# Performance work log

Measured on AMD Instinct MI355X. Metric: run time of the kernel, lower is better.

## Reference

```python
import jax, jax.numpy as jnp
import numpy as np

PAST = 15        # sum(num_classes[:-1])
NC = 20          # sum(num_classes)
ALPHA = 0.99
IGNORE = 255


def setup_inputs() -> dict:
    key = jax.random.key(0)
    k1, k2, k3, k4, k5, k6 = jax.random.split(key, 6)
    B, C, H, W = 8, NC, 512, 512
    logit = jax.random.normal(k1, (B, C, H, W), dtype=jnp.float32)
    # ema_prob is used as probabilities (gathered & compared to thresholds)
    ema_prob = jax.nn.softmax(jax.random.normal(k2, (B, C, H, W), dtype=jnp.float32), axis=1)
    ema_thresh = jax.random.uniform(k3, (NC,), dtype=jnp.float32, minval=0.2, maxval=0.8)
    real_labels = jax.random.randint(k4, (B, H, W), 0, NC, dtype=jnp.int64)
    # sprinkle ignore pixels (255) like real segmentation masks
    real_labels = jnp.where(jax.random.uniform(k5, (B, H, W)) < 0.1, IGNORE, real_labels)
    moving_prob_avg = jax.random.uniform(k6, (NC,), dtype=jnp.float32)
    return {"logit": logit, "ema_prob": ema_prob, "ema_thresh": ema_thresh,
            "real_labels": real_labels, "moving_prob_avg": moving_prob_avg}


def reference(logit, ema_prob, ema_thresh, real_labels, moving_prob_avg):
    # --- pseudo-labels from current model (detached softmax) ---
    logit_prob = jax.nn.softmax(jax.lax.stop_gradient(logit), axis=1)  # [B,C,H,W]
    labels = jnp.argmax(logit_prob[:, :PAST], axis=1)                   # [B,H,W]
    labels = jnp.where(real_labels >= PAST, real_labels, labels)
    idx = jnp.where(real_labels == IGNORE, 0, labels)
    scores = jnp.take_along_axis(logit_prob, idx[:, None], axis=1)[:, 0]  # [B,H,W]

    # --- per-class mean of scores + EMA update of moving_prob_avg ---
    flat_lab = labels.reshape(-1)
    flat_sc = scores.reshape(-1)
    seg = jnp.where(flat_lab == IGNORE, NC, flat_lab)  # route ignored to extra bucket
    sums = jax.ops.segment_sum(flat_sc, seg, num_segments=NC + 1)[:NC]
    counts = jax.ops.segment_sum(jnp.ones_like(flat_sc), seg, num_segments=NC + 1)[:NC]
    means = sums / jnp.maximum(counts, 1.0)
    mpa = moving_prob_avg  # numpy buffer in torch (no grad)
    new_mpa = jnp.where(counts > 0,
                        jnp.where(mpa == -1.0, means, (1.0 - ALPHA) * means + ALPHA * mpa),
                        mpa)

    # --- EMA-teacher pseudo labels + threshold mask ---
    ema_labels = jnp.argmax(ema_prob[:, :PAST], axis=1)
    ema_labels = jnp.where(real_labels >= PAST, real_labels, ema_labels)
    eidx = jnp.where(real_labels == IGNORE, 0, ema_labels)
    ema_scores = jnp.take_along_axis(ema_prob, eidx[:, None], axis=1)[:, 0]
    valid_cls = ema_labels < NC  # 255 never matches any class in the torch loop
    thr = ema_thresh[jnp.clip(ema_labels, 0, NC - 1)]
    ema_mask = valid_cls & (ema_scores >= thr)
    dynamic_labels = jnp.where(ema_mask, ema_labels, IGNORE)  # [B,H,W]

    # --- masked cross-entropy with per-class reweighting ---
    logp = jax.nn.log_softmax(logit, axis=1)
    cidx = jnp.clip(dynamic_labels, 0, NC - 1)
    losses = -jnp.take_along_axis(logp, cidx[:, None], axis=1)[:, 0]
    valid = dynamic_labels != IGNORE
    mult = jnp.where(valid, 1.0 - new_mpa[cidx], 1.0)
    losses = losses * jax.lax.stop_gradient(mult)  # multiplier is a host scalar in torch
    vs = valid.astype(losses.dtype)
    return jnp.sum(losses * vs) / jnp.sum(vs)
```

## Files before the change

### kernel.cpp

```cpp
#include <hip/hip_runtime.h>
#include <math.h>


#define PASTC 15
#define NCC   20
#define IGN   255
#define HW2   262144
#define ALPHAF 0.99f
#define DPF   4

__device__ __forceinline__ void gld_lds16(const float* g, void* l) {
    __builtin_amdgcn_global_load_lds(
        (const __attribute__((address_space(1))) void*)g,
        (__attribute__((address_space(3))) void*)l,
        16, 0, 0);
}

__global__ __launch_bounds__(256) void dl_main(
    const float* __restrict__ logit,
    const float* __restrict__ ema,
    const float* __restrict__ thresh,
    const int*   __restrict__ real,
    float*       __restrict__ ws)
{
    __shared__ float4 s_e[DPF][256];
    __shared__ float4 s_l[DPF][256];
    __shared__ float  s_acc[61];
    __shared__ float  s_thr[NCC];

    const int tid = threadIdx.x;
    if (tid < 61) s_acc[tid] = 0.0f;
    if (tid < NCC) s_thr[tid] = thresh[tid];
    __syncthreads();

    const int t  = blockIdx.x * 256 + tid;
    const int p0 = t << 2;
    const int b  = p0 >> 18;
    const int s  = p0 & (HW2 - 1);
    const size_t base = (((size_t)(b * NCC)) << 18) + (size_t)s;
    const float* eb = ema   + base;
    const float* lb = logit + base;
    const int wbase = tid & ~63;

    const int4 rl4 = *reinterpret_cast<const int4*>(real + p0);
    const int rl[4] = {rl4.x, rl4.y, rl4.z, rl4.w};

    int   cap_ch[4];
    float se[4], x_m15[4], esel[4], xsel[4];
    int   arg15[4], earg[4];
#pragma unroll
    for (int j = 0; j < 4; ++j) {
        cap_ch[j] = (rl[j] == IGN) ? 0 : (rl[j] >= PASTC ? rl[j] : -1);
        se[j] = 0.0f; x_m15[j] = -INFINITY; esel[j] = -INFINITY;
        xsel[j] = 0.0f; arg15[j] = 0; earg[j] = 0;
    }

#pragma unroll
    for (int c = 0; c < DPF; ++c) {
        gld_lds16(eb + ((size_t)c << 18), &s_e[c][wbase]);
        gld_lds16(lb + ((size_t)c << 18), &s_l[c][wbase]);
    }

#pragma unroll
    for (int c = 0; c < NCC; ++c) {
        const int slot = c & (DPF - 1);
        const int vm = (c + DPF < NCC) ? 2 * (DPF - 1) : 2 * (NCC - 1 - c);
        asm volatile("s_waitcnt vmcnt(%0)" :: "n"(vm) : "memory");
        __builtin_amdgcn_sched_barrier(0);

        const float4 ve4 = s_e[slot][tid];
        const float4 vl4 = s_l[slot][tid];
        const float ev[4] = {ve4.x, ve4.y, ve4.z, ve4.w};
        const float xv[4] = {vl4.x, vl4.y, vl4.z, vl4.w};
#pragma unroll
        for (int j = 0; j < 4; ++j) {
            const float x = xv[j];
            se[j] += __expf(x);
            if (c < PASTC) {
                const bool gl = x > x_m15[j];
                x_m15[j] = gl ? x : x_m15[j];
                arg15[j] = gl ? c : arg15[j];
            }
            const bool upd = (cap_ch[j] < 0)
                               ? (c < PASTC && ev[j] > esel[j])
                               : (c == cap_ch[j]);
            esel[j] = upd ? ev[j] : esel[j];
            earg[j] = upd ? c    : earg[j];
            xsel[j] = upd ? x    : xsel[j];
        }

        if (c + DPF < NCC) {
            gld_lds16(eb + ((size_t)(c + DPF) << 18), &s_e[slot][wbase]);
            gld_lds16(lb + ((size_t)(c + DPF) << 18), &s_l[slot][wbase]);
        }
    }

    float vcnt = 0.0f;
#pragma unroll
    for (int j = 0; j < 4; ++j) {
        const float lse = __logf(se[j]);
        if (rl[j] != IGN) {
            const int   lab  = (rl[j] >= PASTC) ? rl[j] : arg15[j];
            const float sval = (rl[j] >= PASTC) ? xsel[j] : x_m15[j];
            const float prob = __expf(sval - lse);
            atomicAdd(&s_acc[lab], prob);
            atomicAdd(&s_acc[20 + lab], 1.0f);
        }
        const int  el    = (rl[j] >= PASTC) ? rl[j] : earg[j];
        const float th   = s_thr[el < NCC ? el : (NCC - 1)];
        const bool valid = (el < NCC) && (esel[j] >= th);
        if (valid) {
            atomicAdd(&s_acc[40 + el], lse - xsel[j]);
        }
        const unsigned long long bm = __ballot(valid);
        if ((tid & 63) == 0) vcnt += (float)__popcll(bm);
    }
    if ((tid & 63) == 0) atomicAdd(&s_acc[60], vcnt);

    __syncthreads();
    if (tid < 61) atomicAdd(&ws[tid], s_acc[tid]);
}

__global__ void dl_final(const float* __restrict__ ws,
                         const float* __restrict__ mpa,
                         float*       __restrict__ out)
{
    if (threadIdx.x == 0 && blockIdx.x == 0) {
        float acc = 0.0f;
        for (int c = 0; c < NCC; ++c) {
            const float ssum = ws[c];
            const float cnt  = ws[20 + c];
            const float lsum = ws[40 + c];
            const float m    = mpa[c];
            const float mean = ssum / fmaxf(cnt, 1.0f);
            const float nm   = (cnt > 0.0f)
                                 ? ((m == -1.0f) ? mean
                                                 : (1.0f - ALPHAF) * mean + ALPHAF * m)
                                 : m;
            acc += lsum * (1.0f - nm);
        }
        out[0] = acc / ws[60];
    }
}

extern "C" void kernel_launch(void* const* d_in, const int* in_sizes, int n_in,
                              void* d_out, int out_size, void* d_ws, size_t ws_size,
                              hipStream_t stream) {
    const float* logit  = (const float*)d_in[0];
    const float* ema    = (const float*)d_in[1];
    const float* thresh = (const float*)d_in[2];
    const int*   real   = (const int*)d_in[3];
    const float* mpa    = (const float*)d_in[4];
    float* out = (float*)d_out;
    float* ws  = (float*)d_ws;

    hipMemsetAsync(ws, 0, 64 * sizeof(float), stream);

    dl_main<<<2048, 256, 0, stream>>>(logit, ema, thresh, real, ws);
    dl_final<<<1, 64, 0, stream>>>(ws, mpa, out);
}
```

Baseline: 364.5 us.

## Split ema and logit passes with direct vector loads, drop LDS prefetch pipeline

Replaces the hand-built global_load_lds ring buffer, which interleaved ema and logit channels, with two sequential passes of plain float4 global loads. The first pass computes the ema argmax and selected value. The second computes the logit sum-exp, argmax and selected logit using the known ema label. Labels and ema scores are parked in LDS to cut register pressure, and launch bounds request 8 blocks per CU. The goal is higher occupancy so the compiler and hardware can hide memory latency with more waves. The cost is losing the explicit prefetch depth.

```diff
diff --git a/kernel.cpp b/kernel.cpp
--- a/kernel.cpp
+++ b/kernel.cpp
@@ -7,26 +7,18 @@
 #define IGN   255
 #define HW2   262144
 #define ALPHAF 0.99f
-#define DPF   4
 
-__device__ __forceinline__ void gld_lds16(const float* g, void* l) {
-    __builtin_amdgcn_global_load_lds(
-        (const __attribute__((address_space(1))) void*)g,
-        (__attribute__((address_space(3))) void*)l,
-        16, 0, 0);
-}
-
-__global__ __launch_bounds__(256) void dl_main(
+__global__ __launch_bounds__(256, 8) void dl_main(
     const float* __restrict__ logit,
     const float* __restrict__ ema,
     const float* __restrict__ thresh,
     const int*   __restrict__ real,
     float*       __restrict__ ws)
 {
-    __shared__ float4 s_e[DPF][256];
-    __shared__ float4 s_l[DPF][256];
     __shared__ float  s_acc[61];
     __shared__ float  s_thr[NCC];
+    __shared__ int4   s_rl[256];
+    __shared__ float4 s_es[256];
 
     const int tid = threadIdx.x;
     if (tid < 61) s_acc[tid] = 0.0f;
@@ -40,75 +32,94 @@
     const size_t base = (((size_t)(b * NCC)) << 18) + (size_t)s;
     const float* eb = ema   + base;
     const float* lb = logit + base;
-    const int wbase = tid & ~63;
 
     const int4 rl4 = *reinterpret_cast<const int4*>(real + p0);
+    s_rl[tid] = rl4;
     const int rl[4] = {rl4.x, rl4.y, rl4.z, rl4.w};
 
-    int   cap_ch[4];
-    float se[4], x_m15[4], esel[4], xsel[4];
-    int   arg15[4], earg[4];
+    int   cap[4], earg[4];
+    float esel[4];
 #pragma unroll
     for (int j = 0; j < 4; ++j) {
-        cap_ch[j] = (rl[j] == IGN) ? 0 : (rl[j] >= PASTC ? rl[j] : -1);
-        se[j] = 0.0f; x_m15[j] = -INFINITY; esel[j] = -INFINITY;
-        xsel[j] = 0.0f; arg15[j] = 0; earg[j] = 0;
+        cap[j]  = (rl[j] == IGN) ? 0 : (rl[j] >= PASTC ? rl[j] : -1);
+        esel[j] = -INFINITY; earg[j] = 0;
     }
 
 #pragma unroll
-    for (int c = 0; c < DPF; ++c) {
-        gld_lds16(eb + ((size_t)c << 18), &s_e[c][wbase]);
-        gld_lds16(lb + ((size_t)c << 18), &s_l[c][wbase]);
+    for (int c = 0; c < PASTC; ++c) {
+        const float4 v = *reinterpret_cast<const float4*>(eb + ((size_t)c << 18));
+        const float ev[4] = {v.x, v.y, v.z, v.w};
+#pragma unroll
+        for (int j = 0; j < 4; ++j) {
+            const bool upd = (cap[j] < 0) ? (ev[j] > esel[j]) : (c == cap[j]);
+            esel[j] = upd ? ev[j] : esel[j];
+            earg[j] = upd ? c     : earg[j];
+        }
     }
+#pragma unroll
+    for (int c = PASTC; c < NCC; ++c) {
+        const float4 v = *reinterpret_cast<const float4*>(eb + ((size_t)c << 18));
+        const float ev[4] = {v.x, v.y, v.z, v.w};
+#pragma unroll
+        for (int j = 0; j < 4; ++j) {
+            const bool upd = (c == cap[j]);
+            esel[j] = upd ? ev[j] : esel[j];
+            earg[j] = upd ? c     : earg[j];
+        }
+    }
+    s_es[tid] = make_float4(esel[0], esel[1], esel[2], esel[3]);
 
+    float se[4], x_m15[4], xsel[4];
+    int   arg15[4];
 #pragma unroll
-    for (int c = 0; c < NCC; ++c) {
-        const int slot = c & (DPF - 1);
-        const int vm = (c + DPF < NCC) ? 2 * (DPF - 1) : 2 * (NCC - 1 - c);
-        asm volatile("s_waitcnt vmcnt(%0)" :: "n"(vm) : "memory");
-        __builtin_amdgcn_sched_barrier(0);
-
-        const float4 ve4 = s_e[slot][tid];
-        const float4 vl4 = s_l[slot][tid];
-        const float ev[4] = {ve4.x, ve4.y, ve4.z, ve4.w};
-        const float xv[4] = {vl4.x, vl4.y, vl4.z, vl4.w};
+    for (int j = 0; j < 4; ++j) {
+        se[j] = 0.0f; x_m15[j] = -INFINITY; xsel[j] = 0.0f; arg15[j] = 0;
+    }
+#pragma unroll
+    for (int c = 0; c < PASTC; ++c) {
+        const float4 v = *reinterpret_cast<const float4*>(lb + ((size_t)c << 18));
+        const float xv[4] = {v.x, v.y, v.z, v.w};
 #pragma unroll
         for (int j = 0; j < 4; ++j) {
             const float x = xv[j];
             se[j] += __expf(x);
-            if (c < PASTC) {
-                const bool gl = x > x_m15[j];
-                x_m15[j] = gl ? x : x_m15[j];
-                arg15[j] = gl ? c : arg15[j];
-            }
-            const bool upd = (cap_ch[j] < 0)
-                               ? (c < PASTC && ev[j] > esel[j])
-                               : (c == cap_ch[j]);
-            esel[j] = upd ? ev[j] : esel[j];
-            earg[j] = upd ? c    : earg[j];
-            xsel[j] = upd ? x    : xsel[j];
-        }
-
-        if (c + DPF < NCC) {
-            gld_lds16(eb + ((size_t)(c + DPF) << 18), &s_e[slot][wbase]);
-            gld_lds16(lb + ((size_t)(c + DPF) << 18), &s_l[slot][wbase]);
+            const bool gl = x > x_m15[j];
+            x_m15[j] = gl ? x : x_m15[j];
+            arg15[j] = gl ? c : arg15[j];
+            xsel[j]  = (c == earg[j]) ? x : xsel[j];
         }
     }
+#pragma unroll
+    for (int c = PASTC; c < NCC; ++c) {
+        const float4 v = *reinterpret_cast<const float4*>(lb + ((size_t)c << 18));
+        const float xv[4] = {v.x, v.y, v.z, v.w};
+#pragma unroll
+        for (int j = 0; j < 4; ++j) {
+            const float x = xv[j];
+            se[j] += __expf(x);
+            xsel[j] = (c == earg[j]) ? x : xsel[j];
+        }
+    }
+
+    const int4   rr4 = s_rl[tid];
+    const float4 ee4 = s_es[tid];
+    const int   rrl[4] = {rr4.x, rr4.y, rr4.z, rr4.w};
+    const float ees[4] = {ee4.x, ee4.y, ee4.z, ee4.w};
 
     float vcnt = 0.0f;
 #pragma unroll
     for (int j = 0; j < 4; ++j) {
         const float lse = __logf(se[j]);
-        if (rl[j] != IGN) {
-            const int   lab  = (rl[j] >= PASTC) ? rl[j] : arg15[j];
-            const float sval = (rl[j] >= PASTC) ? xsel[j] : x_m15[j];
+        if (rrl[j] != IGN) {
+            const int   lab  = (rrl[j] >= PASTC) ? rrl[j] : arg15[j];
+            const float sval = (rrl[j] >= PASTC) ? xsel[j] : x_m15[j];
             const float prob = __expf(sval - lse);
             atomicAdd(&s_acc[lab], prob);
             atomicAdd(&s_acc[20 + lab], 1.0f);
         }
-        const int  el    = (rl[j] >= PASTC) ? rl[j] : earg[j];
+        const int  el    = (rrl[j] >= PASTC) ? rrl[j] : earg[j];
         const float th   = s_thr[el < NCC ? el : (NCC - 1)];
-        const bool valid = (el < NCC) && (esel[j] >= th);
+        const bool valid = (el < NCC) && (ees[j] >= th);
         if (valid) {
             atomicAdd(&s_acc[40 + el], lse - xsel[j]);
         }
```

Result: slower. 448.8 us (+23.1%).
